# Kernel optimization log

Measured on AMD Instinct MI355X. Metric: run time of the kernel, lower is better.

Reference implementation:

```python
import jax, jax.numpy as jnp
import numpy as np

N = 100000
E = 1600000
D = 128
EPS = 1e-5


def setup_inputs() -> dict:
    key = jax.random.key(0)
    ks = jax.random.split(key, 8)
    s = 1.0 / np.sqrt(D)
    feats = jax.random.normal(ks[0], (N, D), dtype=jnp.float32)
    src = jax.random.randint(ks[1], (E,), 0, N, dtype=jnp.int32)
    dst = jax.random.randint(ks[2], (E,), 0, N, dtype=jnp.int32)
    W_gcn = jax.random.normal(ks[3], (D, D), dtype=jnp.float32) * s
    b_gcn = jnp.zeros((D,), dtype=jnp.float32)
    W_res = jax.random.normal(ks[4], (D, D), dtype=jnp.float32) * s
    b_res = jnp.zeros((D,), dtype=jnp.float32)
    g1 = jnp.ones((D,), dtype=jnp.float32)
    be1 = jnp.zeros((D,), dtype=jnp.float32)
    g2 = jnp.ones((D,), dtype=jnp.float32)
    be2 = jnp.zeros((D,), dtype=jnp.float32)
    return {"feats": feats, "W_gcn": W_gcn, "b_gcn": b_gcn, "W_res": W_res,
            "b_res": b_res, "g1": g1, "be1": be1, "g2": g2, "be2": be2,
            "src": src, "dst": dst}


def _batchnorm(x, gamma, beta):
    # BatchNorm1d, training mode: biased batch stats over the node dim
    mu = jnp.mean(x, axis=0)
    var = jnp.var(x, axis=0)
    return gamma * (x - mu) * jax.lax.rsqrt(var + EPS) + beta


def reference(feats, W_gcn, b_gcn, W_res, b_res, g1, be1, g2, be2, src, dst):
    n = feats.shape[0]
    # GraphConv(norm='none'): sum-aggregate neighbor feats then linear (in<=out)
    agg = jax.ops.segment_sum(feats[src], dst, num_segments=n)  # [N, D]
    h = jax.nn.relu(agg @ W_gcn + b_gcn)
    # dgllife GCNLayer internal residual: activation(Linear(feats))
    res = jax.nn.relu(feats @ W_res + b_res)
    h = _batchnorm(h + res, g1, be1)
    # outer ResidualGCNLayer: Identity residual (in_feats==out_feats) + BN
    out = _batchnorm(h + feats, g2, be2)
    return out
```

## Files before the change

### kernel.cpp

```cpp
#include <hip/hip_runtime.h>
#include <hip/hip_bf16.h>
#include <stdint.h>

#define NN 100000
#define EE 1600000
#define DD 128
#define EPSV 1e-5f
#define WWIN 128
#define NB 782
#define NCLS 8
#define NSEG (NB * NCLS)
#define ITEMS (EE / 4)
#define ITEMS_PER_CLS (ITEMS / NCLS)
#define SORTCAP 4096

typedef __attribute__((ext_vector_type(8))) short short8;
typedef __attribute__((ext_vector_type(4))) float floatx4;
typedef unsigned short u16;

union S8 { short8 v; short s[8]; unsigned short u[8]; };

__device__ __forceinline__ float bf2f(u16 u) {
    return __uint_as_float(((unsigned int)u) << 16);
}
__device__ __forceinline__ u16 f2bf(float f) {
    unsigned int x = __float_as_uint(f);
    x += 0x7FFFu + ((x >> 16) & 1u);
    return (u16)(x >> 16);
}


__global__ __launch_bounds__(256) void k_convert(
    const float* __restrict__ ff,
    const float* __restrict__ Wg, const float* __restrict__ Wr,
    const float* __restrict__ bg, const float* __restrict__ br,
    const float* __restrict__ g1, const float* __restrict__ g2,
    const float* __restrict__ be2,
    u16* __restrict__ fc, u16* __restrict__ pc,
    int* __restrict__ flag, int* __restrict__ done,
    int* __restrict__ cnt, float* __restrict__ stats)
{
    const int bx = blockIdx.x;
    const int tx = threadIdx.x;
    if (bx < 27) {
        const int idx = bx * 256 + tx;
        if (idx < 5 * DD) stats[idx] = 0.f;
        else {
            const int j = idx - 5 * DD;
            if (j < NSEG) cnt[j] = 0;
            else if (j == NSEG) *done = 0;
        }
        return;
    }
    __shared__ int dc;
    if (tx == 0) dc = 0;
    __syncthreads();
    const float dv = fabsf(ff[tx]);
    if (dv > 1e-3f && dv < 1e3f) atomicAdd(&dc, 1);
    __syncthreads();
    const int myflag = (dc >= 128) ? 1 : 0;
    if (bx == 27 && tx == 0) *flag = myflag;
    if (!myflag) return;

    if (bx < 158) {
        const int i = (bx - 27) * 256 + tx;
        if (i >= 33408) return;
        float v;
        if (i < 16384)      v = Wg[i];
        else if (i < 32768) v = Wr[i - 16384];
        else {
            const int j = i - 32768;
            const int a = j >> 7, o = j & 127;
            v = (a == 0) ? bg[o] : (a == 1) ? br[o] : (a == 2) ? g1[o]
              : (a == 3) ? g2[o] : be2[o];
        }
        pc[i] = f2bf(v);
        return;
    }
    const int bid = bx - 158;
    const size_t P = (size_t)NN * (DD / 4);
    for (size_t i = (size_t)bid * 256 + tx; i < P; i += (size_t)1024 * 256) {
        const float4 v = *(const float4*)(ff + 4 * i);
        uint2 o;
        o.x = (unsigned int)f2bf(v.x) | ((unsigned int)f2bf(v.y) << 16);
        o.y = (unsigned int)f2bf(v.z) | ((unsigned int)f2bf(v.w) << 16);
        *(uint2*)(fc + 4 * i) = o;
    }
}

__global__ __launch_bounds__(256) void k_hist2(
    const int* __restrict__ dst, int* __restrict__ cnt)
{
    __shared__ int lc[NB];
    const int cls  = blockIdx.x & 7;
    const int blk  = blockIdx.x >> 3;
    const int nblk = gridDim.x >> 3;
    const int it0  = cls * ITEMS_PER_CLS;
    const int it1  = it0 + ITEMS_PER_CLS;
    for (int i = threadIdx.x; i < NB; i += 256) lc[i] = 0;
    __syncthreads();
    const int4* __restrict__ dst4 = (const int4*)dst;
    for (int it = it0 + blk * blockDim.x + threadIdx.x; it < it1;
         it += nblk * blockDim.x) {
        const int4 d = dst4[it];
        atomicAdd(&lc[d.x >> 7], 1);
        atomicAdd(&lc[d.y >> 7], 1);
        atomicAdd(&lc[d.z >> 7], 1);
        atomicAdd(&lc[d.w >> 7], 1);
    }
    __syncthreads();
    for (int i = threadIdx.x; i < NB; i += 256) {
        const int v = lc[i];
        if (v) atomicAdd(&cnt[i * NCLS + cls], v);
    }
}

__global__ __launch_bounds__(1024) void k_scanseg(
    const int* __restrict__ cnt, int* __restrict__ off,
    int* __restrict__ cursor)
{
    const int tx = threadIdx.x;
    const int lane = tx & 63, w = tx >> 6;
    __shared__ int wsum[16];
    __shared__ int carry;
    if (tx == 0) carry = 0;
    __syncthreads();
    for (int base = 0; base < NSEG; base += 1024) {
        const int i = base + tx;
        const int v = (i < NSEG) ? cnt[i] : 0;
        int incl = v;
#pragma unroll
        for (int d = 1; d < 64; d <<= 1) {
            const int n = __shfl_up(incl, d, 64);
            if (lane >= d) incl += n;
        }
        if (lane == 63) wsum[w] = incl;
        __syncthreads();
        if (tx < 16) {
            int s = wsum[tx];
#pragma unroll
            for (int d = 1; d < 16; d <<= 1) {
                const int n = __shfl_up(s, d, 16);
                if ((tx & 15) >= d) s += n;
            }
            wsum[tx] = s;
        }
        __syncthreads();
        const int c = carry;
        const int woff = (w == 0) ? 0 : wsum[w - 1];
        if (i < NSEG) {
            const int excl = c + woff + incl - v;
            off[i] = excl;
            cursor[i] = excl;
        }
        __syncthreads();
        if (tx == 0) carry = c + wsum[15];
        __syncthreads();
    }
    if (tx == 0) off[NSEG] = carry;
}

__global__ __launch_bounds__(256) void k_bin(
    const int* __restrict__ src, const int* __restrict__ dst,
    int* __restrict__ cursor, unsigned int* __restrict__ arena)
{
    __shared__ int lc[NB], lb[NB];
    const int cls  = blockIdx.x & 7;
    const int blk  = blockIdx.x >> 3;
    const int nblk = gridDim.x >> 3;
    const int it0  = cls * ITEMS_PER_CLS;
    const int it1  = it0 + ITEMS_PER_CLS;
    const int4* __restrict__ dst4 = (const int4*)dst;
    const int4* __restrict__ src4 = (const int4*)src;
    for (int i = threadIdx.x; i < NB; i += 256) lc[i] = 0;
    __syncthreads();
    for (int it = it0 + blk * blockDim.x + threadIdx.x; it < it1;
         it += nblk * blockDim.x) {
        const int4 d = dst4[it];
        atomicAdd(&lc[d.x >> 7], 1);
        atomicAdd(&lc[d.y >> 7], 1);
        atomicAdd(&lc[d.z >> 7], 1);
        atomicAdd(&lc[d.w >> 7], 1);
    }
    __syncthreads();
    for (int i = threadIdx.x; i < NB; i += 256) {
        const int v = lc[i];
        lb[i] = v ? atomicAdd(&cursor[i * NCLS + cls], v) : 0;
    }
    __syncthreads();
    for (int i = threadIdx.x; i < NB; i += 256) lc[i] = 0;
    __syncthreads();
    for (int it = it0 + blk * blockDim.x + threadIdx.x; it < it1;
         it += nblk * blockDim.x) {
        const int4 d = dst4[it];
        const int4 s = src4[it];
        int wv, p;
        wv = d.x >> 7; p = lb[wv] + atomicAdd(&lc[wv], 1);
        arena[p] = ((unsigned int)(d.x & 127) << 17) | (unsigned int)s.x;
        wv = d.y >> 7; p = lb[wv] + atomicAdd(&lc[wv], 1);
        arena[p] = ((unsigned int)(d.y & 127) << 17) | (unsigned int)s.y;
        wv = d.z >> 7; p = lb[wv] + atomicAdd(&lc[wv], 1);
        arena[p] = ((unsigned int)(d.z & 127) << 17) | (unsigned int)s.z;
        wv = d.w >> 7; p = lb[wv] + atomicAdd(&lc[wv], 1);
        arena[p] = ((unsigned int)(d.w & 127) << 17) | (unsigned int)s.w;
    }
}

__global__ __launch_bounds__(256) void k_sortgather(
    const int* __restrict__ flag,
    const u16* __restrict__ feats_raw, const u16* __restrict__ feats_c,
    const unsigned int* __restrict__ arena, const int* __restrict__ off,
    u16* __restrict__ aggb)
{
    __shared__ unsigned int buf[SORTCAP];
    __shared__ int sorted[SORTCAP];
    __shared__ int cnt_[WWIN], pref[WWIN], cur[WWIN];
    const u16* __restrict__ F = (*flag != 0) ? feats_c : feats_raw;
    const int tx = threadIdx.x;
    const int b  = blockIdx.x;
    const int s0 = off[b * NCLS];
    int len = off[b * NCLS + NCLS] - s0;
    if (len > SORTCAP) len = SORTCAP;
    if (tx < WWIN) cnt_[tx] = 0;
    __syncthreads();
    for (int i = tx; i < len; i += 256) {
        const unsigned int p = arena[s0 + i];
        buf[i] = p;
        atomicAdd(&cnt_[p >> 17], 1);
    }
    __syncthreads();
    if (tx < WWIN) pref[tx] = cnt_[tx];
    __syncthreads();
    for (int d = 1; d < WWIN; d <<= 1) {
        int v = 0;
        if (tx < WWIN && tx >= d) v = pref[tx - d];
        __syncthreads();
        if (tx < WWIN) pref[tx] += v;
        __syncthreads();
    }
    if (tx < WWIN) cur[tx] = pref[tx] - cnt_[tx];
    __syncthreads();
    for (int i = tx; i < len; i += 256) {
        const unsigned int p = buf[i];
        const int pos = atomicAdd(&cur[p >> 17], 1);
        sorted[pos] = (int)(p & 0x1FFFFu);
    }
    __syncthreads();

    const int lane = tx & 63;
    const int l16  = lane & 15;
    const int wv   = tx >> 6;
    for (int it = 0; it < 8; ++it) {
        const int nloc = wv * 32 + it * 4 + (lane >> 4);
        const int node = b * WWIN + nloc;
        const int deg  = cnt_[nloc];
        const int rs   = pref[nloc] - deg;
        float a0 = 0.f, a1 = 0.f, a2 = 0.f, a3 = 0.f;
        float a4 = 0.f, a5 = 0.f, a6 = 0.f, a7 = 0.f;
        int j = 0;
        for (; j + 8 <= deg; j += 8) {
            uint4 vv[8];
#pragma unroll
            for (int q = 0; q < 8; ++q) {
                const int s = sorted[rs + j + q];
                vv[q] = *(const uint4*)(F + (size_t)s * DD + l16 * 8);
            }
#pragma unroll
            for (int q = 0; q < 8; ++q) {
                a0 += bf2f((u16)(vv[q].x & 0xFFFFu));
                a1 += bf2f((u16)(vv[q].x >> 16));
                a2 += bf2f((u16)(vv[q].y & 0xFFFFu));
                a3 += bf2f((u16)(vv[q].y >> 16));
                a4 += bf2f((u16)(vv[q].z & 0xFFFFu));
                a5 += bf2f((u16)(vv[q].z >> 16));
                a6 += bf2f((u16)(vv[q].w & 0xFFFFu));
                a7 += bf2f((u16)(vv[q].w >> 16));
            }
        }
        for (; j < deg; ++j) {
            const int s = sorted[rs + j];
            const uint4 v = *(const uint4*)(F + (size_t)s * DD + l16 * 8);
            a0 += bf2f((u16)(v.x & 0xFFFFu));
            a1 += bf2f((u16)(v.x >> 16));
            a2 += bf2f((u16)(v.y & 0xFFFFu));
            a3 += bf2f((u16)(v.y >> 16));
            a4 += bf2f((u16)(v.z & 0xFFFFu));
            a5 += bf2f((u16)(v.z >> 16));
            a6 += bf2f((u16)(v.w & 0xFFFFu));
            a7 += bf2f((u16)(v.w >> 16));
        }
        if (node < NN) {
            uint4 o;
            o.x = (unsigned int)f2bf(a0) | ((unsigned int)f2bf(a1) << 16);
            o.y = (unsigned int)f2bf(a2) | ((unsigned int)f2bf(a3) << 16);
            o.z = (unsigned int)f2bf(a4) | ((unsigned int)f2bf(a5) << 16);
            o.w = (unsigned int)f2bf(a6) | ((unsigned int)f2bf(a7) << 16);
            *(uint4*)(aggb + (size_t)node * DD + l16 * 8) = o;
        }
    }
}

__global__ __launch_bounds__(256) void k_gemm(
    const int* __restrict__ flag,
    const u16* __restrict__ aggb,
    const u16* __restrict__ feats_raw, const u16* __restrict__ feats_c,
    const u16* __restrict__ Wg_raw, const u16* __restrict__ bg_raw,
    const u16* __restrict__ Wr_raw, const u16* __restrict__ br_raw,
    const u16* __restrict__ pc,
    u16* __restrict__ t_out, float* __restrict__ stats)
{
    const bool f32 = (*flag != 0);
    const u16* __restrict__ F  = f32 ? feats_c     : feats_raw;
    const u16* __restrict__ Wg = f32 ? pc          : Wg_raw;
    const u16* __restrict__ Wr = f32 ? pc + 16384  : Wr_raw;
    const u16* __restrict__ bg = f32 ? pc + 32768  : bg_raw;
    const u16* __restrict__ br = f32 ? pc + 32896  : br_raw;

    const int lane = threadIdx.x & 63;
    const int wv   = threadIdx.x >> 6;
    const int l15  = lane & 15;
    const int quad = lane >> 4;
    const int c0 = wv * 16 + l15;
    const int c1 = 64 + wv * 16 + l15;

    S8 fg0[4], fg1[4], fr0[4], fr1[4];
#pragma unroll
    for (int kb = 0; kb < 4; ++kb) {
        const int kr = kb * 32 + quad * 8;
#pragma unroll
        for (int j = 0; j < 8; ++j) {
            fg0[kb].u[j] = Wg[(size_t)(kr + j) * DD + c0];
            fg1[kb].u[j] = Wg[(size_t)(kr + j) * DD + c1];
            fr0[kb].u[j] = Wr[(size_t)(kr + j) * DD + c0];
            fr1[kb].u[j] = Wr[(size_t)(kr + j) * DD + c1];
        }
    }
    const float bgc0 = bf2f(bg[c0]), bgc1 = bf2f(bg[c1]);
    const float brc0 = bf2f(br[c0]), brc1 = bf2f(br[c1]);

    float s_t0 = 0.f, s_t1 = 0.f, s_tt0 = 0.f, s_tt1 = 0.f;
    float s_f0 = 0.f, s_f1 = 0.f, s_ff0 = 0.f, s_ff1 = 0.f;
    float s_tf0 = 0.f, s_tf1 = 0.f;

    for (int tile = blockIdx.x; tile < NN / 16; tile += gridDim.x) {
        const int row0 = tile * 16;
        const int arow = row0 + l15;
        floatx4 ag0 = {0.f,0.f,0.f,0.f}, ag1 = {0.f,0.f,0.f,0.f};
        floatx4 ar0 = {0.f,0.f,0.f,0.f}, ar1 = {0.f,0.f,0.f,0.f};
#pragma unroll
        for (int kb = 0; kb < 4; ++kb) {
            const int kbase = kb * 32 + quad * 8;
            S8 av, ff;
            av.v = *(const short8*)(aggb + (size_t)arow * DD + kbase);
            ff.v = *(const short8*)(F    + (size_t)arow * DD + kbase);
            ag0 = __builtin_amdgcn_mfma_f32_16x16x32_bf16(av.v, fg0[kb].v, ag0, 0, 0, 0);
            ag1 = __builtin_amdgcn_mfma_f32_16x16x32_bf16(av.v, fg1[kb].v, ag1, 0, 0, 0);
            ar0 = __builtin_amdgcn_mfma_f32_16x16x32_bf16(ff.v, fr0[kb].v, ar0, 0, 0, 0);
            ar1 = __builtin_amdgcn_mfma_f32_16x16x32_bf16(ff.v, fr1[kb].v, ar1, 0, 0, 0);
        }
#pragma unroll
        for (int r = 0; r < 4; ++r) {
            const int row = row0 + quad * 4 + r;
            const u16 tb0 = f2bf(fmaxf(ag0[r] + bgc0, 0.f) + fmaxf(ar0[r] + brc0, 0.f));
            const u16 tb1 = f2bf(fmaxf(ag1[r] + bgc1, 0.f) + fmaxf(ar1[r] + brc1, 0.f));
            t_out[(size_t)row * DD + c0] = tb0;
            t_out[(size_t)row * DD + c1] = tb1;
            const float t0 = bf2f(tb0), t1 = bf2f(tb1);
            const float fv0 = bf2f(F[(size_t)row * DD + c0]);
            const float fv1 = bf2f(F[(size_t)row * DD + c1]);
            s_t0  += t0;        s_t1  += t1;
            s_tt0 += t0 * t0;   s_tt1 += t1 * t1;
            s_f0  += fv0;       s_f1  += fv1;
            s_ff0 += fv0 * fv0; s_ff1 += fv1 * fv1;
            s_tf0 += t0 * fv0;  s_tf1 += t1 * fv1;
        }
    }

#define QRED(x) x += __shfl_xor(x, 16, 64); x += __shfl_xor(x, 32, 64);
    QRED(s_t0)  QRED(s_t1)  QRED(s_tt0) QRED(s_tt1)
    QRED(s_f0)  QRED(s_f1)  QRED(s_ff0) QRED(s_ff1)
    QRED(s_tf0) QRED(s_tf1)
#undef QRED
    if (quad == 0) {
        unsafeAtomicAdd(&stats[0 * DD + c0], s_t0);
        unsafeAtomicAdd(&stats[0 * DD + c1], s_t1);
        unsafeAtomicAdd(&stats[1 * DD + c0], s_tt0);
        unsafeAtomicAdd(&stats[1 * DD + c1], s_tt1);
        unsafeAtomicAdd(&stats[2 * DD + c0], s_f0);
        unsafeAtomicAdd(&stats[2 * DD + c1], s_f1);
        unsafeAtomicAdd(&stats[3 * DD + c0], s_ff0);
        unsafeAtomicAdd(&stats[3 * DD + c1], s_ff1);
        unsafeAtomicAdd(&stats[4 * DD + c0], s_tf0);
        unsafeAtomicAdd(&stats[4 * DD + c1], s_tf1);
    }
}

__global__ __launch_bounds__(256) void k_final(
    const int* __restrict__ flag,
    const u16* __restrict__ t,
    const u16* __restrict__ feats_raw, const u16* __restrict__ feats_c,
    const u16* __restrict__ g1_raw, const u16* __restrict__ g2_raw,
    const u16* __restrict__ be2_raw, const u16* __restrict__ pc,
    const float* __restrict__ stats,
    void* __restrict__ out)
{
    const bool f32 = (*flag != 0);
    const u16* __restrict__ F   = f32 ? feats_c    : feats_raw;
    const u16* __restrict__ g1  = f32 ? pc + 33024 : g1_raw;
    const u16* __restrict__ g2  = f32 ? pc + 33152 : g2_raw;
    const u16* __restrict__ be2 = f32 ? pc + 33280 : be2_raw;

    __shared__ float sA[DD], sB[DD], sG[DD];
    if (threadIdx.x < DD) {
        const int c = threadIdx.x;
        const float invN = 1.0f / (float)NN;
        const float St  = stats[c],          Stt = stats[DD + c];
        const float Sf  = stats[2 * DD + c], Sff = stats[3 * DD + c];
        const float Stf = stats[4 * DD + c];
        const float mu1  = St * invN;
        const float vart = fmaxf(Stt * invN - mu1 * mu1, 0.f);
        const float muf  = Sf * invN;
        const float varf = fmaxf(Sff * invN - muf * muf, 0.f);
        const float cov  = Stf * invN - mu1 * muf;
        const float r1   = rsqrtf(vart + EPSV);
        const float a1   = bf2f(g1[c]) * r1;
        const float var2 = fmaxf(a1 * a1 * vart + 2.f * a1 * cov + varf, 0.f);
        const float r2   = rsqrtf(var2 + EPSV);
        const float g2r2 = bf2f(g2[c]) * r2;
        sA[c] = g2r2 * a1;
        sB[c] = g2r2;
        sG[c] = bf2f(be2[c]) - g2r2 * (a1 * mu1 + muf);
    }
    __syncthreads();

    float* outf = (float*)out;
    u16*   outb = (u16*)out;
    const size_t P = (size_t)NN * (DD / 4);
    for (size_t i = (size_t)blockIdx.x * blockDim.x + threadIdx.x; i < P;
         i += (size_t)gridDim.x * blockDim.x) {
        const int c = ((int)(i & 31)) * 4;
        const uint2 tv = *(const uint2*)(t + 4 * i);
        const uint2 fv = *(const uint2*)(F + 4 * i);
        const float o0 = sA[c]     * bf2f((u16)(tv.x & 0xFFFFu))
                       + sB[c]     * bf2f((u16)(fv.x & 0xFFFFu)) + sG[c];
        const float o1 = sA[c + 1] * bf2f((u16)(tv.x >> 16))
                       + sB[c + 1] * bf2f((u16)(fv.x >> 16)) + sG[c + 1];
        const float o2 = sA[c + 2] * bf2f((u16)(tv.y & 0xFFFFu))
                       + sB[c + 2] * bf2f((u16)(fv.y & 0xFFFFu)) + sG[c + 2];
        const float o3 = sA[c + 3] * bf2f((u16)(tv.y >> 16))
                       + sB[c + 3] * bf2f((u16)(fv.y >> 16)) + sG[c + 3];
        if (f32) {
            float4 o; o.x = o0; o.y = o1; o.z = o2; o.w = o3;
            *(float4*)(outf + 4 * i) = o;
        } else {
            uint2 ov;
            ov.x = (unsigned int)f2bf(o0) | ((unsigned int)f2bf(o1) << 16);
            ov.y = (unsigned int)f2bf(o2) | ((unsigned int)f2bf(o3) << 16);
            *(uint2*)(outb + 4 * i) = ov;
        }
    }
}

extern "C" void kernel_launch(void* const* d_in, const int* in_sizes, int n_in,
                              void* d_out, int out_size, void* d_ws, size_t ws_size,
                              hipStream_t stream) {
    const u16* feats = (const u16*)d_in[0];
    const u16* Wg    = (const u16*)d_in[1];
    const u16* bg    = (const u16*)d_in[2];
    const u16* Wr    = (const u16*)d_in[3];
    const u16* br    = (const u16*)d_in[4];
    const u16* g1    = (const u16*)d_in[5];
    const u16* g2    = (const u16*)d_in[7];
    const u16* be2   = (const u16*)d_in[8];
    const int* src = (const int*)d_in[9];
    const int* dst = (const int*)d_in[10];

    char* ws = (char*)d_ws;
    u16*          aggb    = (u16*)  ws;
    u16*          t       = (u16*)  (ws + 25600000);
    u16*          feats_c = (u16*)  (ws + 51200000);
    u16*          pc      = (u16*)  (ws + 76800000);
    float*        stats   = (float*)(ws + 76866816);
    int*          flag    = (int*)  (ws + 76869376);
    int*          done    = (int*)  (ws + 76869380);
    int*          cnt     = (int*)  (ws + 76869632);
    int*          off     = (int*)  (ws + 76894656);
    int*          cursor  = (int*)  (ws + 76919684);
    unsigned int* arena   = (unsigned int*)(ws + 77344712);

    k_convert<<<1182, 256, 0, stream>>>((const float*)d_in[0],
        (const float*)d_in[1], (const float*)d_in[3], (const float*)d_in[2],
        (const float*)d_in[4], (const float*)d_in[5], (const float*)d_in[7],
        (const float*)d_in[8], feats_c, pc, flag, done, cnt, stats);

    k_hist2     <<<256, 256, 0, stream>>>(dst, cnt);
    k_scanseg   <<<1, 1024, 0, stream>>>(cnt, off, cursor);
    k_bin       <<<256, 256, 0, stream>>>(src, dst, cursor, arena);
    k_sortgather<<<NB, 256, 0, stream>>>(flag, feats, feats_c, arena, off, aggb);
    k_gemm      <<<1024, 256, 0, stream>>>(flag, aggb, feats, feats_c, Wg, bg, Wr, br, pc, t, stats);
    k_final     <<<2048, 256, 0, stream>>>(flag, t, feats, feats_c, g1, g2, be2, pc, stats, d_out);
}
```

Baseline: 289.5 us.

## Fuse neighbor gather-aggregate with dual GEMM via shared-memory aggregate tile

Merges the sort/gather kernel and the GEMM kernel so that each block aggregates its 128-node window into a padded LDS tile and then runs the MFMA GEMMs directly from it. This removes the global write and re-read of the bf16 aggregate buffer and one kernel launch. In exchange, the per-block weight fragment loads now happen in 782 blocks, the sort buffer is replaced by rereading the arena from global memory, and the larger LDS footprint may lower occupancy.

```diff
diff --git a/kernel.cpp b/kernel.cpp
--- a/kernel.cpp
+++ b/kernel.cpp
@@ -13,6 +13,7 @@
 #define ITEMS (EE / 4)
 #define ITEMS_PER_CLS (ITEMS / NCLS)
 #define SORTCAP 4096
+#define AGS 136
 
 typedef __attribute__((ext_vector_type(8))) short short8;
 typedef __attribute__((ext_vector_type(4))) float floatx4;
@@ -206,28 +207,36 @@
     }
 }
 
-__global__ __launch_bounds__(256) void k_sortgather(
+__global__ __launch_bounds__(256) void k_sgg(
     const int* __restrict__ flag,
     const u16* __restrict__ feats_raw, const u16* __restrict__ feats_c,
     const unsigned int* __restrict__ arena, const int* __restrict__ off,
-    u16* __restrict__ aggb)
-{
-    __shared__ unsigned int buf[SORTCAP];
+    const u16* __restrict__ Wg_raw, const u16* __restrict__ bg_raw,
+    const u16* __restrict__ Wr_raw, const u16* __restrict__ br_raw,
+    const u16* __restrict__ pc,
+    u16* __restrict__ t_out, float* __restrict__ stats)
+{
     __shared__ int sorted[SORTCAP];
+    __shared__ u16 aggL[WWIN * AGS];
     __shared__ int cnt_[WWIN], pref[WWIN], cur[WWIN];
-    const u16* __restrict__ F = (*flag != 0) ? feats_c : feats_raw;
+
+    const bool f32 = (*flag != 0);
+    const u16* __restrict__ F  = f32 ? feats_c     : feats_raw;
+    const u16* __restrict__ Wg = f32 ? pc          : Wg_raw;
+    const u16* __restrict__ Wr = f32 ? pc + 16384  : Wr_raw;
+    const u16* __restrict__ bg = f32 ? pc + 32768  : bg_raw;
+    const u16* __restrict__ br = f32 ? pc + 32896  : br_raw;
+
     const int tx = threadIdx.x;
     const int b  = blockIdx.x;
     const int s0 = off[b * NCLS];
     int len = off[b * NCLS + NCLS] - s0;
     if (len > SORTCAP) len = SORTCAP;
+
     if (tx < WWIN) cnt_[tx] = 0;
     __syncthreads();
-    for (int i = tx; i < len; i += 256) {
-        const unsigned int p = arena[s0 + i];
-        buf[i] = p;
-        atomicAdd(&cnt_[p >> 17], 1);
-    }
+    for (int i = tx; i < len; i += 256)
+        atomicAdd(&cnt_[arena[s0 + i] >> 17], 1);
     __syncthreads();
     if (tx < WWIN) pref[tx] = cnt_[tx];
     __syncthreads();
@@ -241,7 +250,7 @@
     if (tx < WWIN) cur[tx] = pref[tx] - cnt_[tx];
     __syncthreads();
     for (int i = tx; i < len; i += 256) {
-        const unsigned int p = buf[i];
+        const unsigned int p = arena[s0 + i];
         const int pos = atomicAdd(&cur[p >> 17], 1);
         sorted[pos] = (int)(p & 0x1FFFFu);
     }
@@ -252,7 +261,6 @@
     const int wv   = tx >> 6;
     for (int it = 0; it < 8; ++it) {
         const int nloc = wv * 32 + it * 4 + (lane >> 4);
-        const int node = b * WWIN + nloc;
         const int deg  = cnt_[nloc];
         const int rs   = pref[nloc] - deg;
         float a0 = 0.f, a1 = 0.f, a2 = 0.f, a3 = 0.f;
@@ -289,35 +297,15 @@
             a6 += bf2f((u16)(v.w & 0xFFFFu));
             a7 += bf2f((u16)(v.w >> 16));
         }
-        if (node < NN) {
-            uint4 o;
-            o.x = (unsigned int)f2bf(a0) | ((unsigned int)f2bf(a1) << 16);
-            o.y = (unsigned int)f2bf(a2) | ((unsigned int)f2bf(a3) << 16);
-            o.z = (unsigned int)f2bf(a4) | ((unsigned int)f2bf(a5) << 16);
-            o.w = (unsigned int)f2bf(a6) | ((unsigned int)f2bf(a7) << 16);
-            *(uint4*)(aggb + (size_t)node * DD + l16 * 8) = o;
-        }
-    }
-}
-
-__global__ __launch_bounds__(256) void k_gemm(
-    const int* __restrict__ flag,
-    const u16* __restrict__ aggb,
-    const u16* __restrict__ feats_raw, const u16* __restrict__ feats_c,
-    const u16* __restrict__ Wg_raw, const u16* __restrict__ bg_raw,
-    const u16* __restrict__ Wr_raw, const u16* __restrict__ br_raw,
-    const u16* __restrict__ pc,
-    u16* __restrict__ t_out, float* __restrict__ stats)
-{
-    const bool f32 = (*flag != 0);
-    const u16* __restrict__ F  = f32 ? feats_c     : feats_raw;
-    const u16* __restrict__ Wg = f32 ? pc          : Wg_raw;
-    const u16* __restrict__ Wr = f32 ? pc + 16384  : Wr_raw;
-    const u16* __restrict__ bg = f32 ? pc + 32768  : bg_raw;
-    const u16* __restrict__ br = f32 ? pc + 32896  : br_raw;
-
-    const int lane = threadIdx.x & 63;
-    const int wv   = threadIdx.x >> 6;
+        uint4 o;
+        o.x = (unsigned int)f2bf(a0) | ((unsigned int)f2bf(a1) << 16);
+        o.y = (unsigned int)f2bf(a2) | ((unsigned int)f2bf(a3) << 16);
+        o.z = (unsigned int)f2bf(a4) | ((unsigned int)f2bf(a5) << 16);
+        o.w = (unsigned int)f2bf(a6) | ((unsigned int)f2bf(a7) << 16);
+        *(uint4*)(aggL + nloc * AGS + l16 * 8) = o;
+    }
+    __syncthreads();
+
     const int l15  = lane & 15;
     const int quad = lane >> 4;
     const int c0 = wv * 16 + l15;
@@ -342,17 +330,19 @@
     float s_f0 = 0.f, s_f1 = 0.f, s_ff0 = 0.f, s_ff1 = 0.f;
     float s_tf0 = 0.f, s_tf1 = 0.f;
 
-    for (int tile = blockIdx.x; tile < NN / 16; tile += gridDim.x) {
-        const int row0 = tile * 16;
-        const int arow = row0 + l15;
+    const int node0 = b * WWIN;
+    for (int tile = 0; tile < 8; ++tile) {
+        const int row0 = node0 + tile * 16;
+        if (row0 >= NN) break;
+        const int arow_l = tile * 16 + l15;
         floatx4 ag0 = {0.f,0.f,0.f,0.f}, ag1 = {0.f,0.f,0.f,0.f};
         floatx4 ar0 = {0.f,0.f,0.f,0.f}, ar1 = {0.f,0.f,0.f,0.f};
 #pragma unroll
         for (int kb = 0; kb < 4; ++kb) {
             const int kbase = kb * 32 + quad * 8;
             S8 av, ff;
-            av.v = *(const short8*)(aggb + (size_t)arow * DD + kbase);
-            ff.v = *(const short8*)(F    + (size_t)arow * DD + kbase);
+            av.v = *(const short8*)(aggL + arow_l * AGS + kbase);
+            ff.v = *(const short8*)(F + (size_t)(node0 + arow_l) * DD + kbase);
             ag0 = __builtin_amdgcn_mfma_f32_16x16x32_bf16(av.v, fg0[kb].v, ag0, 0, 0, 0);
             ag1 = __builtin_amdgcn_mfma_f32_16x16x32_bf16(av.v, fg1[kb].v, ag1, 0, 0, 0);
             ar0 = __builtin_amdgcn_mfma_f32_16x16x32_bf16(ff.v, fr0[kb].v, ar0, 0, 0, 0);
@@ -476,7 +466,6 @@
     const int* dst = (const int*)d_in[10];
 
     char* ws = (char*)d_ws;
-    u16*          aggb    = (u16*)  ws;
     u16*          t       = (u16*)  (ws + 25600000);
     u16*          feats_c = (u16*)  (ws + 51200000);
     u16*          pc      = (u16*)  (ws + 76800000);
@@ -493,10 +482,10 @@
         (const float*)d_in[4], (const float*)d_in[5], (const float*)d_in[7],
         (const float*)d_in[8], feats_c, pc, flag, done, cnt, stats);
 
-    k_hist2     <<<256, 256, 0, stream>>>(dst, cnt);
-    k_scanseg   <<<1, 1024, 0, stream>>>(cnt, off, cursor);
-    k_bin       <<<256, 256, 0, stream>>>(src, dst, cursor, arena);
-    k_sortgather<<<NB, 256, 0, stream>>>(flag, feats, feats_c, arena, off, aggb);
-    k_gemm      <<<1024, 256, 0, stream>>>(flag, aggb, feats, feats_c, Wg, bg, Wr, br, pc, t, stats);
-    k_final     <<<2048, 256, 0, stream>>>(flag, t, feats, feats_c, g1, g2, be2, pc, stats, d_out);
-}
+    k_hist2  <<<256, 256, 0, stream>>>(dst, cnt);
+    k_scanseg<<<1, 1024, 0, stream>>>(cnt, off, cursor);
+    k_bin    <<<256, 256, 0, stream>>>(src, dst, cursor, arena);
+    k_sgg    <<<NB, 256, 0, stream>>>(flag, feats, feats_c, arena, off,
+                                      Wg, bg, Wr, br, pc, t, stats);
+    k_final  <<<2048, 256, 0, stream>>>(flag, t, feats, feats_c, g1, g2, be2, pc, stats, d_out);
+}
```

New measurement: 287.2 us. About the same (-0.8%).
